# Performance work log

Measured on AMD Instinct MI355X. Metric: run time of the kernel, lower is better.

## Reference

```python
import jax, jax.numpy as jnp
import numpy as np

N_STATE = 1024
N_HEAD = 16
B = 2
S = 2048


def setup_inputs() -> dict:
    key = jax.random.key(0)
    ks = jax.random.split(key, 8)
    s = 0.02
    x = jax.random.normal(ks[0], (B, S, N_STATE), dtype=jnp.float32)
    # causal additive mask, as in Whisper: upper triangle = -inf
    mask = jnp.where(jnp.triu(jnp.ones((S, S), dtype=bool), k=1), -jnp.inf, 0.0).astype(jnp.float32)
    Wq = jax.random.normal(ks[1], (N_STATE, N_STATE), dtype=jnp.float32) * s
    bq = jax.random.normal(ks[2], (N_STATE,), dtype=jnp.float32) * s
    Wk = jax.random.normal(ks[3], (N_STATE, N_STATE), dtype=jnp.float32) * s
    Wv = jax.random.normal(ks[4], (N_STATE, N_STATE), dtype=jnp.float32) * s
    bv = jax.random.normal(ks[5], (N_STATE,), dtype=jnp.float32) * s
    Wo = jax.random.normal(ks[6], (N_STATE, N_STATE), dtype=jnp.float32) * s
    bo = jax.random.normal(ks[7], (N_STATE,), dtype=jnp.float32) * s
    return {"x": x, "mask": mask, "Wq": Wq, "bq": bq, "Wk": Wk,
            "Wv": Wv, "bv": bv, "Wo": Wo, "bo": bo}


def reference(x, mask, Wq, bq, Wk, Wv, bv, Wo, bo):
    Bb, S_, D = x.shape
    H = N_HEAD
    hd = D // H
    scale = hd ** (-0.25)  # scale split across q and k, as in the source
    q = x @ Wq.T + bq              # [B,S,D]
    k = x @ Wk.T                   # key has no bias
    v = x @ Wv.T + bv
    # [B,S,D] -> [B,H,S,hd]
    q = q.reshape(Bb, S_, H, hd).transpose(0, 2, 1, 3) * scale
    k = k.reshape(Bb, S_, H, hd).transpose(0, 2, 1, 3) * scale
    v = v.reshape(Bb, S_, H, hd).transpose(0, 2, 1, 3)
    qk = jnp.einsum('bhsd,bhtd->bhst', q, k) + mask[:S_, :S_]
    w = jax.nn.softmax(qk, axis=-1).astype(q.dtype)
    out = jnp.einsum('bhst,bhtd->bhsd', w, v)
    out = out.transpose(0, 2, 1, 3).reshape(Bb, S_, D)
    return out @ Wo.T + bo
```

## Files before the change

### kernel.cpp

```cpp
#include <hip/hip_runtime.h>
#include <hip/hip_bf16.h>
#include <cmath>

typedef __bf16 bf16;
typedef __bf16 bf16x8 __attribute__((ext_vector_type(8)));
typedef __bf16 bf16x4 __attribute__((ext_vector_type(4)));
typedef float f32x4 __attribute__((ext_vector_type(4)));

#define QS 0.18033688f

__device__ __forceinline__ void load16_to_lds(const void* g, void* l) {
    __builtin_amdgcn_global_load_lds(
        (const __attribute__((address_space(1))) unsigned int*)g,
        (__attribute__((address_space(3))) unsigned int*)l, 16, 0, 0);
}

__global__ __launch_bounds__(256) void convert_kernel(
    const float* __restrict__ x,  const float* __restrict__ wq,
    const float* __restrict__ wk, const float* __restrict__ wv,
    const float* __restrict__ wo, bf16* __restrict__ dst)
{
    const size_t M1 = 1024ull * 1024ull, M4 = 4ull * M1;
    size_t i0 = ((size_t)blockIdx.x * 256 + threadIdx.x) * 8;
    const float* s;
    size_t off;
    float sc = 1.f;
    if      (i0 < M4)        { s = x;  off = i0; }
    else if (i0 < M4 + M1)   { s = wq; off = i0 - M4; sc = QS; }
    else if (i0 < M4 + 2*M1) { s = wk; off = i0 - M4 - M1; }
    else if (i0 < M4 + 3*M1) { s = wv; off = i0 - M4 - 2*M1; }
    else                     { s = wo; off = i0 - M4 - 3*M1; }
    float4 a = *(const float4*)(s + off);
    float4 b = *(const float4*)(s + off + 4);
    bf16x8 r = { (bf16)(a.x*sc), (bf16)(a.y*sc), (bf16)(a.z*sc), (bf16)(a.w*sc),
                 (bf16)(b.x*sc), (bf16)(b.y*sc), (bf16)(b.z*sc), (bf16)(b.w*sc) };
    *(bf16x8*)(dst + i0) = r;
}

template<int BM, bool OUT_F32>
__device__ __forceinline__ void gemm_core(
    const bf16* __restrict__ A, const bf16* __restrict__ W,
    const float* __restrict__ bias, void* __restrict__ C,
    int mb, int nb, bool vt_out, float bias_scale)
{
    constexpr int IF = BM / 32;
    __shared__ __align__(16) bf16 As[BM * 32];
    __shared__ __align__(16) bf16 Bs[128 * 32];

    const int tid  = threadIdx.x;
    const int lane = tid & 63;
    const int wave = tid >> 6;
    const int wr   = (wave >> 1) * (BM / 2);
    const int wc   = (wave & 1) * 64;
    const int l15  = lane & 15;
    const int l4   = lane >> 4;
    const int swz  = (l4 ^ ((l15 >> 1) & 3)) * 8;

    f32x4 acc[IF][4] = {};

    for (int kt = 0; kt < 32; ++kt) {
#pragma unroll
        for (int it = 0; it < BM / 64; ++it) {
            int c = it * 256 + tid;
            int scol = ((c & 3) ^ ((c >> 3) & 3)) * 8;
            load16_to_lds(&A[(size_t)(mb * BM + (c >> 2)) * 1024 + kt * 32 + scol],
                          &As[(it * 256 + (tid & 192)) * 8]);
        }
#pragma unroll
        for (int it = 0; it < 2; ++it) {
            int c = it * 256 + tid;
            int scol = ((c & 3) ^ ((c >> 3) & 3)) * 8;
            load16_to_lds(&W[(size_t)(nb * 128 + (c >> 2)) * 1024 + kt * 32 + scol],
                          &Bs[(it * 256 + (tid & 192)) * 8]);
        }
        __syncthreads();
        bf16x8 af[IF], bfr[4];
#pragma unroll
        for (int i = 0; i < IF; ++i)
            af[i] = *(const bf16x8*)&As[(wr + i * 16 + l15) * 32 + swz];
#pragma unroll
        for (int j = 0; j < 4; ++j)
            bfr[j] = *(const bf16x8*)&Bs[(wc + j * 16 + l15) * 32 + swz];
#pragma unroll
        for (int i = 0; i < IF; ++i)
#pragma unroll
            for (int j = 0; j < 4; ++j)
                acc[i][j] = __builtin_amdgcn_mfma_f32_16x16x32_bf16(
                    af[i], bfr[j], acc[i][j], 0, 0, 0);
        __syncthreads();
    }

    if (!OUT_F32 && vt_out) {
#pragma unroll
        for (int j = 0; j < 4; ++j) {
            int col = nb * 128 + wc + j * 16 + l15;
            float bv = bias ? bias[col] : 0.f;
            int h = col >> 6, d = col & 63;
#pragma unroll
            for (int i = 0; i < IF; ++i) {
                int m0 = mb * BM + wr + i * 16 + l4 * 4;
                int b = m0 >> 11, s = m0 & 2047;
                bf16x4 pk = { (bf16)(acc[i][j][0] + bv), (bf16)(acc[i][j][1] + bv),
                              (bf16)(acc[i][j][2] + bv), (bf16)(acc[i][j][3] + bv) };
                *(bf16x4*)&((bf16*)C)[(size_t)((b * 16 + h) * 64 + d) * 2048 + s] = pk;
            }
        }
    } else {
#pragma unroll
        for (int j = 0; j < 4; ++j) {
            int col = nb * 128 + wc + j * 16 + l15;
            float bv = bias ? bias[col] * bias_scale : 0.f;
#pragma unroll
            for (int i = 0; i < IF; ++i) {
                int row0 = mb * BM + wr + i * 16 + l4 * 4;
#pragma unroll
                for (int r = 0; r < 4; ++r) {
                    float val = acc[i][j][r] + bv;
                    size_t idx = (size_t)(row0 + r) * 1024 + col;
                    if (OUT_F32) ((float*)C)[idx] = val;
                    else         ((bf16*)C)[idx]  = (bf16)val;
                }
            }
        }
    }
}

__global__ __launch_bounds__(256) void qkv_kernel(
    const bf16* __restrict__ xb,
    const bf16* __restrict__ wqb, const float* __restrict__ bq,
    const bf16* __restrict__ wkb,
    const bf16* __restrict__ wvb, const float* __restrict__ bv,
    bf16* __restrict__ q, bf16* __restrict__ k, bf16* __restrict__ vt)
{
    int mb = blockIdx.x;
    int nbg = blockIdx.y;
    int sel = nbg >> 3, nb = nbg & 7;
    const bf16* W = (sel == 0) ? wqb : ((sel == 1) ? wkb : wvb);
    const float* bias = (sel == 0) ? bq : ((sel == 2) ? bv : nullptr);
    bf16* C = (sel == 0) ? q : ((sel == 1) ? k : vt);
    gemm_core<128, false>(xb, W, bias, C, mb, nb, sel == 2,
                          sel == 0 ? QS : 1.f);
}

__global__ __launch_bounds__(256) void oproj_kernel(
    const bf16* __restrict__ ao, const bf16* __restrict__ wob,
    const float* __restrict__ bo, float* __restrict__ out)
{
    gemm_core<64, true>(ao, wob, bo, out, blockIdx.x, blockIdx.y, false, 1.f);
}

__global__ __launch_bounds__(256) void attn_kernel(
    const bf16* __restrict__ q, const bf16* __restrict__ k,
    const bf16* __restrict__ vt, bf16* __restrict__ o)
{
    __shared__ __align__(16) bf16 Ks[2][64 * 64];
    __shared__ __align__(16) bf16 Vs[2][64 * 64];
    __shared__ __align__(16) bf16 Ps[4][16 * 72];

    const int tid  = threadIdx.x;
    const int lane = tid & 63;
    const int wave = tid >> 6;
    const int l15  = lane & 15;
    const int l4   = lane >> 4;

    const int qt = 31 - blockIdx.x;
    const int bh = blockIdx.y;
    const int b = bh >> 4, h = bh & 15;

    auto stage = [&](int nt, int buf) {
#pragma unroll
        for (int it = 0; it < 2; ++it) {
            int c = it * 256 + tid;
            int scol = ((c & 7) ^ ((c >> 3) & 7)) * 8;
            load16_to_lds(&k[(size_t)(b * 2048 + nt * 64 + (c >> 3)) * 1024 + h * 64 + scol],
                          &Ks[buf][(it * 256 + (tid & 192)) * 8]);
            load16_to_lds(&vt[(size_t)(bh * 64 + (c >> 3)) * 2048 + nt * 64 + scol],
                          &Vs[buf][(it * 256 + (tid & 192)) * 8]);
        }
    };

    const int qg = qt * 64 + wave * 16 + l15;
    bf16x8 qf[2];
#pragma unroll
    for (int kk = 0; kk < 2; ++kk)
        qf[kk] = *(const bf16x8*)&q[(size_t)(b * 2048 + qg) * 1024 + h * 64 + kk * 32 + l4 * 8];

    f32x4 oacc[4] = {};
    float lsum = 0.f;
    int b0 = 0;
    stage(0, 0);

    for (int nt = 0; nt <= qt; ++nt) {
        __syncthreads();
        if (nt < qt) stage(nt + 1, b0 ^ 1);

        f32x4 s[4] = {};
#pragma unroll
        for (int kk = 0; kk < 2; ++kk) {
#pragma unroll
            for (int j = 0; j < 4; ++j) {
                bf16x8 kf = *(const bf16x8*)&Ks[b0][(j * 16 + l15) * 64
                                + (((kk * 4 + l4) ^ (l15 & 7)) * 8)];
                s[j] = __builtin_amdgcn_mfma_f32_16x16x32_bf16(kf, qf[kk], s[j], 0, 0, 0);
            }
        }

        float pv[4][4];
        if (nt == qt) {
#pragma unroll
            for (int j = 0; j < 4; ++j)
#pragma unroll
                for (int r = 0; r < 4; ++r) {
                    int kg = nt * 64 + j * 16 + l4 * 4 + r;
                    pv[j][r] = (kg > qg) ? 0.f : __builtin_amdgcn_exp2f(s[j][r]);
                }
        } else {
#pragma unroll
            for (int j = 0; j < 4; ++j)
#pragma unroll
                for (int r = 0; r < 4; ++r)
                    pv[j][r] = __builtin_amdgcn_exp2f(s[j][r]);
        }
#pragma unroll
        for (int j = 0; j < 4; ++j)
            lsum += (pv[j][0] + pv[j][1]) + (pv[j][2] + pv[j][3]);

#pragma unroll
        for (int j = 0; j < 4; ++j) {
            bf16x4 pk = { (bf16)pv[j][0], (bf16)pv[j][1], (bf16)pv[j][2], (bf16)pv[j][3] };
            *(bf16x4*)&Ps[wave][l15 * 72 + j * 16 + l4 * 4] = pk;
        }

#pragma unroll
        for (int kk = 0; kk < 2; ++kk) {
            bf16x8 pf = *(const bf16x8*)&Ps[wave][l15 * 72 + kk * 32 + l4 * 8];
#pragma unroll
            for (int f = 0; f < 4; ++f) {
                bf16x8 vf = *(const bf16x8*)&Vs[b0][(f * 16 + l15) * 64
                                + (((kk * 4 + l4) ^ (l15 & 7)) * 8)];
                oacc[f] = __builtin_amdgcn_mfma_f32_16x16x32_bf16(pf, vf, oacc[f], 0, 0, 0);
            }
        }
        b0 ^= 1;
    }

    lsum += __shfl_xor(lsum, 16, 64);
    lsum += __shfl_xor(lsum, 32, 64);
    float rinv[4];
#pragma unroll
    for (int r = 0; r < 4; ++r) rinv[r] = 1.f / __shfl(lsum, l4 * 4 + r, 64);
#pragma unroll
    for (int f = 0; f < 4; ++f)
#pragma unroll
        for (int r = 0; r < 4; ++r)
            o[(size_t)(b * 2048 + qt * 64 + wave * 16 + l4 * 4 + r) * 1024 + h * 64 + f * 16 + l15]
                = (bf16)(oacc[f][r] * rinv[r]);
}

extern "C" void kernel_launch(void* const* d_in, const int* in_sizes, int n_in,
                              void* d_out, int out_size, void* d_ws, size_t ws_size,
                              hipStream_t stream)
{
    const float* x  = (const float*)d_in[0];
    const float* Wq = (const float*)d_in[2];
    const float* bq = (const float*)d_in[3];
    const float* Wk = (const float*)d_in[4];
    const float* Wv = (const float*)d_in[5];
    const float* bv = (const float*)d_in[6];
    const float* Wo = (const float*)d_in[7];
    const float* bo = (const float*)d_in[8];
    float* out = (float*)d_out;

    const size_t M1 = 1024ull * 1024ull, M4 = 4ull * M1;
    bf16* base = (bf16*)d_ws;
    bf16* xb  = base;
    bf16* wqb = base + M4;
    bf16* wkb = base + M4 + M1;
    bf16* wvb = base + M4 + 2 * M1;
    bf16* wob = base + M4 + 3 * M1;
    bf16* q   = base + 8 * M1;
    bf16* k   = base + 12 * M1;
    bf16* vt  = base + 16 * M1;
    bf16* ao  = xb;

    convert_kernel<<<4096, 256, 0, stream>>>(x, Wq, Wk, Wv, Wo, base);
    qkv_kernel<<<dim3(32, 24), 256, 0, stream>>>(xb, wqb, bq, wkb, wvb, bv, q, k, vt);
    attn_kernel<<<dim3(32, 32), 256, 0, stream>>>(q, k, vt, ao);
    oproj_kernel<<<dim3(64, 8), 256, 0, stream>>>(ao, wob, bo, out);
}
```

Measured before the change: 217.8 us.

## Pair causal query tiles in 512-thread blocks sharing K/V staging

Each attention block now runs 8 waves covering two query tiles, pairIdx and 31-pairIdx, so every block walks the same number of key tiles (33 total). This balances the triangular causal workload across blocks and shares one K/V LDS stage between the two tiles, cutting redundant global loads. The grid shrinks to 512 blocks with larger blocks. Waves of the short tile sit idle at barriers until the long tile finishes.

Result: faster. 186.5 us (-14.4%).

```diff
diff --git a/kernel.cpp b/kernel.cpp
--- a/kernel.cpp
+++ b/kernel.cpp
@@ -149,37 +149,37 @@
     gemm_core<64, true>(ao, wob, bo, out, blockIdx.x, blockIdx.y, false, 1.f);
 }
 
-__global__ __launch_bounds__(256) void attn_kernel(
+__global__ __launch_bounds__(512) void attn_kernel(
     const bf16* __restrict__ q, const bf16* __restrict__ k,
     const bf16* __restrict__ vt, bf16* __restrict__ o)
 {
     __shared__ __align__(16) bf16 Ks[2][64 * 64];
     __shared__ __align__(16) bf16 Vs[2][64 * 64];
-    __shared__ __align__(16) bf16 Ps[4][16 * 72];
+    __shared__ __align__(16) bf16 Ps[8][16 * 72];
 
     const int tid  = threadIdx.x;
     const int lane = tid & 63;
     const int wave = tid >> 6;
+    const int wv   = wave & 3;
+    const int grp  = wave >> 2;
     const int l15  = lane & 15;
     const int l4   = lane >> 4;
 
-    const int qt = 31 - blockIdx.x;
-    const int bh = blockIdx.y;
+    const int bh = blockIdx.x;
+    const int pairIdx = blockIdx.y;
     const int b = bh >> 4, h = bh & 15;
+    const int myqt = grp ? (31 - pairIdx) : pairIdx;
+    const int maxN = 32 - pairIdx;
 
     auto stage = [&](int nt, int buf) {
-#pragma unroll
-        for (int it = 0; it < 2; ++it) {
-            int c = it * 256 + tid;
-            int scol = ((c & 7) ^ ((c >> 3) & 7)) * 8;
-            load16_to_lds(&k[(size_t)(b * 2048 + nt * 64 + (c >> 3)) * 1024 + h * 64 + scol],
-                          &Ks[buf][(it * 256 + (tid & 192)) * 8]);
-            load16_to_lds(&vt[(size_t)(bh * 64 + (c >> 3)) * 2048 + nt * 64 + scol],
-                          &Vs[buf][(it * 256 + (tid & 192)) * 8]);
-        }
+        int scol = ((tid & 7) ^ ((tid >> 3) & 7)) * 8;
+        load16_to_lds(&k[(size_t)(b * 2048 + nt * 64 + (tid >> 3)) * 1024 + h * 64 + scol],
+                      &Ks[buf][(tid & 448) * 8]);
+        load16_to_lds(&vt[(size_t)(bh * 64 + (tid >> 3)) * 2048 + nt * 64 + scol],
+                      &Vs[buf][(tid & 448) * 8]);
     };
 
-    const int qg = qt * 64 + wave * 16 + l15;
+    const int qg = myqt * 64 + wv * 16 + l15;
     bf16x8 qf[2];
 #pragma unroll
     for (int kk = 0; kk < 2; ++kk)
@@ -190,55 +190,57 @@
     int b0 = 0;
     stage(0, 0);
 
-    for (int nt = 0; nt <= qt; ++nt) {
+    for (int nt = 0; nt < maxN; ++nt) {
         __syncthreads();
-        if (nt < qt) stage(nt + 1, b0 ^ 1);
-
-        f32x4 s[4] = {};
-#pragma unroll
-        for (int kk = 0; kk < 2; ++kk) {
+        if (nt + 1 < maxN) stage(nt + 1, b0 ^ 1);
+
+        if (nt <= myqt) {
+            f32x4 s[4] = {};
+#pragma unroll
+            for (int kk = 0; kk < 2; ++kk) {
+#pragma unroll
+                for (int j = 0; j < 4; ++j) {
+                    bf16x8 kf = *(const bf16x8*)&Ks[b0][(j * 16 + l15) * 64
+                                    + (((kk * 4 + l4) ^ (l15 & 7)) * 8)];
+                    s[j] = __builtin_amdgcn_mfma_f32_16x16x32_bf16(kf, qf[kk], s[j], 0, 0, 0);
+                }
+            }
+
+            float pv[4][4];
+            if (nt == myqt) {
+#pragma unroll
+                for (int j = 0; j < 4; ++j)
+#pragma unroll
+                    for (int r = 0; r < 4; ++r) {
+                        int kg = nt * 64 + j * 16 + l4 * 4 + r;
+                        pv[j][r] = (kg > qg) ? 0.f : __builtin_amdgcn_exp2f(s[j][r]);
+                    }
+            } else {
+#pragma unroll
+                for (int j = 0; j < 4; ++j)
+#pragma unroll
+                    for (int r = 0; r < 4; ++r)
+                        pv[j][r] = __builtin_amdgcn_exp2f(s[j][r]);
+            }
+#pragma unroll
+            for (int j = 0; j < 4; ++j)
+                lsum += (pv[j][0] + pv[j][1]) + (pv[j][2] + pv[j][3]);
+
 #pragma unroll
             for (int j = 0; j < 4; ++j) {
-                bf16x8 kf = *(const bf16x8*)&Ks[b0][(j * 16 + l15) * 64
-                                + (((kk * 4 + l4) ^ (l15 & 7)) * 8)];
-                s[j] = __builtin_amdgcn_mfma_f32_16x16x32_bf16(kf, qf[kk], s[j], 0, 0, 0);
-            }
-        }
-
-        float pv[4][4];
-        if (nt == qt) {
-#pragma unroll
-            for (int j = 0; j < 4; ++j)
-#pragma unroll
-                for (int r = 0; r < 4; ++r) {
-                    int kg = nt * 64 + j * 16 + l4 * 4 + r;
-                    pv[j][r] = (kg > qg) ? 0.f : __builtin_amdgcn_exp2f(s[j][r]);
+                bf16x4 pk = { (bf16)pv[j][0], (bf16)pv[j][1], (bf16)pv[j][2], (bf16)pv[j][3] };
+                *(bf16x4*)&Ps[wave][l15 * 72 + j * 16 + l4 * 4] = pk;
+            }
+
+#pragma unroll
+            for (int kk = 0; kk < 2; ++kk) {
+                bf16x8 pf = *(const bf16x8*)&Ps[wave][l15 * 72 + kk * 32 + l4 * 8];
+#pragma unroll
+                for (int f = 0; f < 4; ++f) {
+                    bf16x8 vf = *(const bf16x8*)&Vs[b0][(f * 16 + l15) * 64
+                                    + (((kk * 4 + l4) ^ (l15 & 7)) * 8)];
+                    oacc[f] = __builtin_amdgcn_mfma_f32_16x16x32_bf16(pf, vf, oacc[f], 0, 0, 0);
                 }
-        } else {
-#pragma unroll
-            for (int j = 0; j < 4; ++j)
-#pragma unroll
-                for (int r = 0; r < 4; ++r)
-                    pv[j][r] = __builtin_amdgcn_exp2f(s[j][r]);
-        }
-#pragma unroll
-        for (int j = 0; j < 4; ++j)
-            lsum += (pv[j][0] + pv[j][1]) + (pv[j][2] + pv[j][3]);
-
-#pragma unroll
-        for (int j = 0; j < 4; ++j) {
-            bf16x4 pk = { (bf16)pv[j][0], (bf16)pv[j][1], (bf16)pv[j][2], (bf16)pv[j][3] };
-            *(bf16x4*)&Ps[wave][l15 * 72 + j * 16 + l4 * 4] = pk;
-        }
-
-#pragma unroll
-        for (int kk = 0; kk < 2; ++kk) {
-            bf16x8 pf = *(const bf16x8*)&Ps[wave][l15 * 72 + kk * 32 + l4 * 8];
-#pragma unroll
-            for (int f = 0; f < 4; ++f) {
-                bf16x8 vf = *(const bf16x8*)&Vs[b0][(f * 16 + l15) * 64
-                                + (((kk * 4 + l4) ^ (l15 & 7)) * 8)];
-                oacc[f] = __builtin_amdgcn_mfma_f32_16x16x32_bf16(pf, vf, oacc[f], 0, 0, 0);
             }
         }
         b0 ^= 1;
@@ -253,7 +255,7 @@
     for (int f = 0; f < 4; ++f)
 #pragma unroll
         for (int r = 0; r < 4; ++r)
-            o[(size_t)(b * 2048 + qt * 64 + wave * 16 + l4 * 4 + r) * 1024 + h * 64 + f * 16 + l15]
+            o[(size_t)(b * 2048 + myqt * 64 + wv * 16 + l4 * 4 + r) * 1024 + h * 64 + f * 16 + l15]
                 = (bf16)(oacc[f][r] * rinv[r]);
 }
 
@@ -285,6 +287,6 @@
 
     convert_kernel<<<4096, 256, 0, stream>>>(x, Wq, Wk, Wv, Wo, base);
     qkv_kernel<<<dim3(32, 24), 256, 0, stream>>>(xb, wqb, bq, wkb, wvb, bv, q, k, vt);
-    attn_kernel<<<dim3(32, 32), 256, 0, stream>>>(q, k, vt, ao);
+    attn_kernel<<<dim3(32, 16), 512, 0, stream>>>(q, k, vt, ao);
     oproj_kernel<<<dim3(64, 8), 256, 0, stream>>>(ao, wob, bo, out);
 }
```
